# Optimization experiments

Measured on AMD Instinct MI355X. Metric: run time of the kernel, lower is better.

## Reference

```python
import jax, jax.numpy as jnp
import numpy as np

N_NODES = 50000
N_EDGES = 800000
IN_F = 64
HID = 64
N_CLS = 16


def setup_inputs() -> dict:
    key = jax.random.key(0)
    ks = jax.random.split(key, 8)
    x = jax.random.normal(ks[0], (N_NODES, IN_F), dtype=jnp.float32)
    edge_index = jax.random.randint(ks[1], (2, N_EDGES), 0, N_NODES, dtype=jnp.int64)
    s = 1.0 / np.sqrt(IN_F)
    W1_l = jax.random.uniform(ks[2], (IN_F, HID), jnp.float32, -s, s)
    W1_r = jax.random.uniform(ks[3], (IN_F, HID), jnp.float32, -s, s)
    b1 = jnp.zeros((HID,), jnp.float32)
    s2 = 1.0 / np.sqrt(HID)
    W2_l = jax.random.uniform(ks[4], (HID, N_CLS), jnp.float32, -s2, s2)
    W2_r = jax.random.uniform(ks[5], (HID, N_CLS), jnp.float32, -s2, s2)
    b2 = jnp.zeros((N_CLS,), jnp.float32)
    return {"x": x, "edge_index": edge_index, "W1_l": W1_l, "b1": b1, "W1_r": W1_r,
            "W2_l": W2_l, "b2": b2, "W2_r": W2_r}


def _sage_conv(x, src, dst, n_nodes, W_l, b_l, W_r):
    # PyG SAGEConv (aggr='mean'): out = lin_l(mean_j x_j) + lin_r(x_i)
    msg_sum = jax.ops.segment_sum(x[src], dst, num_segments=n_nodes)  # [N, F]
    deg = jax.ops.segment_sum(jnp.ones((src.shape[0],), x.dtype), dst,
                              num_segments=n_nodes)
    mean = msg_sum / jnp.maximum(deg, 1.0)[:, None]
    return mean @ W_l + b_l + x @ W_r


def reference(x, edge_index, W1_l, b1, W1_r, W2_l, b2, W2_r):
    src, dst = edge_index[0], edge_index[1]
    n = x.shape[0]
    h = _sage_conv(x, src, dst, n, W1_l, b1, W1_r)
    h = jax.nn.relu(h)
    # dropout is identity in eval mode
    out = _sage_conv(h, src, dst, n, W2_l, b2, W2_r)
    return out
```

## Files before the change

kernel.cpp:

```cpp
#include <hip/hip_runtime.h>

#define N_NODES 50000
#define N_EDGES 800000
#define NB      391
#define NBP     392
#define G       128
#define SCAN_N  (NBP * G)
#define SCAN_BLOCKS 49
#define MAXB    3072

typedef _Float16 h2v __attribute__((ext_vector_type(2)));
typedef _Float16 h8v __attribute__((ext_vector_type(8)));
typedef float    f4v __attribute__((ext_vector_type(4)));

union H2U { h2v h; unsigned u; };

__global__ void prep_kernel(const float* __restrict__ x,
                            const float* __restrict__ W1_l,
                            const float* __restrict__ W1_r,
                            const float* __restrict__ W2_l,
                            const float* __restrict__ W2_r,
                            _Float16* __restrict__ xf,
                            _Float16* __restrict__ B1,
                            _Float16* __restrict__ B2) {
    const int tid = blockIdx.x * 256 + threadIdx.x;
    {
        float4 v = *(const float4*)(x + tid * 4);
        H2U a, b;
        a.h = h2v{ (_Float16)v.x, (_Float16)v.y };
        b.h = h2v{ (_Float16)v.z, (_Float16)v.w };
        uint2 o = { a.u, b.u };
        *(uint2*)(xf + tid * 4) = o;
    }
    if (blockIdx.x == 0) {
        const int t = threadIdx.x;
        for (int p = t; p < 16 * 512; p += 256) {
            const int frag = p >> 9, lane = (p >> 3) & 63, j = p & 7;
            const int kt = frag >> 2, nt = frag & 3;
            const int k = kt * 32 + (lane >> 4) * 8 + j;
            const int n = nt * 16 + (lane & 15);
            const float w = (k < 64) ? W1_l[k * 64 + n] : W1_r[(k - 64) * 64 + n];
            B1[p] = (_Float16)w;
        }
        for (int p = t; p < 4 * 512; p += 256) {
            const int frag = p >> 9, lane = (p >> 3) & 63, j = p & 7;
            const int kt = frag >> 1, nt = frag & 1;
            const int k = kt * 32 + (lane >> 4) * 8 + j;
            const int n = lane & 15;
            const float w = (nt == 0) ? W2_l[k * 16 + n] : W2_r[k * 16 + n];
            B2[p] = (_Float16)w;
        }
    }
}

__global__ __launch_bounds__(512) void count_kernel(const int* __restrict__ dst,
                                                    int* __restrict__ histG) {
    __shared__ int hist[NBP];
    const int b = blockIdx.x, t = threadIdx.x;
    for (int i = t; i < NBP; i += 512) hist[i] = 0;
    __syncthreads();
    for (int i4 = b * 512 + t; i4 < N_EDGES / 4; i4 += G * 512) {
        int4 d = *(const int4*)(dst + i4 * 4);
        atomicAdd(&hist[d.x >> 7], 1);
        atomicAdd(&hist[d.y >> 7], 1);
        atomicAdd(&hist[d.z >> 7], 1);
        atomicAdd(&hist[d.w >> 7], 1);
    }
    __syncthreads();
    for (int i = t; i < NB; i += 512) histG[b * NBP + i] = hist[i];
}

__global__ void scanA_kernel(const int* __restrict__ histG,
                             int* __restrict__ loc,
                             int* __restrict__ bsum) {
    __shared__ int lds[256];
    const int b = blockIdx.x, t = threadIdx.x;
    const int base = b * 1024 + t * 4;
    int v[4];
    #pragma unroll
    for (int q = 0; q < 4; ++q) {
        const int i = base + q;
        v[q] = histG[(i & (G - 1)) * NBP + (i >> 7)];
    }
    const int s = v[0] + v[1] + v[2] + v[3];
    lds[t] = s;
    __syncthreads();
    for (int off = 1; off < 256; off <<= 1) {
        int u = (t >= off) ? lds[t - off] : 0;
        __syncthreads();
        lds[t] += u;
        __syncthreads();
    }
    const int excl = lds[t] - s;
    int4 o;
    o.x = excl;
    o.y = excl + v[0];
    o.z = excl + v[0] + v[1];
    o.w = excl + v[0] + v[1] + v[2];
    *(int4*)(loc + base) = o;
    if (t == 255) bsum[b] = lds[255];
}

__global__ void scanC_kernel(const int* __restrict__ loc,
                             const int* __restrict__ bsum,
                             int* __restrict__ offT) {
    const int b = blockIdx.x, t = threadIdx.x;
    const int lane = t & 63;
    int v = (lane < SCAN_BLOCKS) ? bsum[lane] : 0;
    for (int off = 1; off < 64; off <<= 1) {
        int u = __shfl_up(v, off);
        if (lane >= off) v += u;
    }
    const int boff = (b == 0) ? 0 : __shfl(v, b - 1);
    const int base = b * 1024 + t * 4;
    int4 w = *(const int4*)(loc + base);
    w.x += boff; w.y += boff; w.z += boff; w.w += boff;
    *(int4*)(offT + base) = w;
}

__global__ __launch_bounds__(512) void scatter_kernel(const int* __restrict__ src,
                                                      const int* __restrict__ dst,
                                                      const int* __restrict__ offT,
                                                      int* __restrict__ bbuf) {
    __shared__ int cur[NB];
    const int b = blockIdx.x, t = threadIdx.x;
    for (int i = t; i < NB; i += 512) cur[i] = offT[i * G + b];
    __syncthreads();
    for (int i4 = b * 512 + t; i4 < N_EDGES / 4; i4 += G * 512) {
        int4 s = *(const int4*)(src + i4 * 4);
        int4 d = *(const int4*)(dst + i4 * 4);
        #pragma unroll
        for (int q = 0; q < 4; ++q) {
            const int dv = (q == 0) ? d.x : (q == 1) ? d.y : (q == 2) ? d.z : d.w;
            const int sv = (q == 0) ? s.x : (q == 1) ? s.y : (q == 2) ? s.z : s.w;
            const int pos = atomicAdd(&cur[dv >> 7], 1);
            bbuf[pos] = ((dv & 127) << 16) | sv;
        }
    }
}

__global__ __launch_bounds__(256) void build_kernel(
        const int* __restrict__ offT,
        const int* __restrict__ bbuf,
        int* __restrict__ csr_src,
        int* __restrict__ rowptr) {
    __shared__ int stash[MAXB];
    __shared__ int lcsr[MAXB];
    __shared__ int hist[128];
    __shared__ int cur[128];

    const int b = blockIdx.x, t = threadIdx.x;
    const int start = offT[b * G];
    const int end = offT[(b + 1) * G];
    const int cnt_b = min(end - start, MAXB);

    if (t < 128) hist[t] = 0;
    __syncthreads();

    for (int i = t; i < cnt_b; i += 256) {
        const int w = bbuf[start + i];
        stash[i] = w;
        atomicAdd(&hist[w >> 16], 1);
    }
    __syncthreads();

    const int orig = (t < 128) ? hist[t] : 0;
    for (int off = 1; off < 128; off <<= 1) {
        int v = (t >= off && t < 128) ? hist[t - off] : 0;
        __syncthreads();
        if (t < 128) hist[t] += v;
        __syncthreads();
    }
    if (t < 128) cur[t] = hist[t] - orig;
    __syncthreads();

    const int node = b * 128 + t;
    if (t < 128 && node < N_NODES) rowptr[node] = start + cur[t];
    if (b == NB - 1 && t == 0) rowptr[N_NODES] = N_EDGES;

    for (int i = t; i < cnt_b; i += 256) {
        const int w = stash[i];
        const int p = atomicAdd(&cur[w >> 16], 1);
        lcsr[p] = w & 0xFFFF;
    }
    __syncthreads();

    for (int i = t; i < cnt_b; i += 256) csr_src[start + i] = lcsr[i];
}

__global__ __launch_bounds__(256) void gather_kernel(
        const _Float16* __restrict__ xf,
        const int* __restrict__ rowptr,
        const int* __restrict__ csr_src,
        _Float16* __restrict__ meanf) {
    const int n = blockIdx.x * 4 + (threadIdx.x >> 6);
    const int l = threadIdx.x & 63;
    const int c = l & 7;
    const int g = l >> 3;

    const int beg = rowptr[n];
    const int end = rowptr[n + 1];
    const int deg = end - beg;
    const int chunk = (deg + 7) >> 3;

    H2U a0, a1, a2, a3;
    a0.u = a1.u = a2.u = a3.u = 0;
    {
        int i = beg + g * chunk;
        const int ce = min(i + chunk, end);
        for (; i + 1 < ce; i += 2) {
            const int p = csr_src[i];
            const int q = csr_src[i + 1];
            uint4 up = *(const uint4*)(xf + p * 64 + c * 8);
            uint4 uq = *(const uint4*)(xf + q * 64 + c * 8);
            H2U t;
            t.u = up.x; a0.h += t.h;  t.u = uq.x; a0.h += t.h;
            t.u = up.y; a1.h += t.h;  t.u = uq.y; a1.h += t.h;
            t.u = up.z; a2.h += t.h;  t.u = uq.z; a2.h += t.h;
            t.u = up.w; a3.h += t.h;  t.u = uq.w; a3.h += t.h;
        }
        if (i < ce) {
            const int p = csr_src[i];
            uint4 up = *(const uint4*)(xf + p * 64 + c * 8);
            H2U t;
            t.u = up.x; a0.h += t.h;
            t.u = up.y; a1.h += t.h;
            t.u = up.z; a2.h += t.h;
            t.u = up.w; a3.h += t.h;
        }
    }
    #pragma unroll
    for (int off = 8; off <= 32; off <<= 1) {
        H2U r;
        r.u = (unsigned)__shfl_xor((int)a0.u, off); a0.h += r.h;
        r.u = (unsigned)__shfl_xor((int)a1.u, off); a1.h += r.h;
        r.u = (unsigned)__shfl_xor((int)a2.u, off); a2.h += r.h;
        r.u = (unsigned)__shfl_xor((int)a3.u, off); a3.h += r.h;
    }
    const float rdeg = 1.0f / fmaxf((float)deg, 1.0f);
    const _Float16 rh = (_Float16)rdeg;
    const h2v rd2 = { rh, rh };
    a0.h *= rd2; a1.h *= rd2; a2.h *= rd2; a3.h *= rd2;
    if (g == 0) {
        uint4 o = { a0.u, a1.u, a2.u, a3.u };
        *(uint4*)(meanf + n * 64 + c * 8) = o;
    }
}

__global__ __launch_bounds__(256) void mlp_kernel(
        const _Float16* __restrict__ xf,
        const _Float16* __restrict__ meanf,
        const _Float16* __restrict__ B1,
        const _Float16* __restrict__ B2,
        const float* __restrict__ b1,
        const float* __restrict__ b2,
        _Float16* __restrict__ y2f,
        float* __restrict__ z) {
    __shared__ _Float16 hlds[4][16 * 72];
    const int widx = threadIdx.x >> 6;
    const int l = threadIdx.x & 63;
    const int n0 = (blockIdx.x * 4 + widx) * 16;
    if (n0 >= N_NODES) return;
    const int cn = l & 15;
    const int kq = l >> 4;

    h8v af[4];
    const _Float16* mrow = meanf + (n0 + cn) * 64 + kq * 8;
    af[0] = *(const h8v*)(mrow);
    af[1] = *(const h8v*)(mrow + 32);
    const _Float16* xrow = xf + (n0 + cn) * 64 + kq * 8;
    af[2] = *(const h8v*)(xrow);
    af[3] = *(const h8v*)(xrow + 32);

    const f4v zero = { 0.f, 0.f, 0.f, 0.f };
    f4v acc[4] = { zero, zero, zero, zero };
    #pragma unroll
    for (int nt = 0; nt < 4; ++nt) {
        #pragma unroll
        for (int kt = 0; kt < 4; ++kt) {
            h8v bf = *(const h8v*)(B1 + ((kt * 4 + nt) * 64 + l) * 8);
            acc[nt] = __builtin_amdgcn_mfma_f32_16x16x32_f16(af[kt], bf, acc[nt], 0, 0, 0);
        }
    }

    _Float16* hl = &hlds[widx][0];
    #pragma unroll
    for (int nt = 0; nt < 4; ++nt) {
        const float bias = b1[nt * 16 + cn];
        #pragma unroll
        for (int r = 0; r < 4; ++r) {
            const float hv = fmaxf(acc[nt][r] + bias, 0.f);
            hl[(kq * 4 + r) * 72 + nt * 16 + cn] = (_Float16)hv;
        }
    }

    h8v a2[2];
    a2[0] = *(const h8v*)(hl + cn * 72 + kq * 8);
    a2[1] = *(const h8v*)(hl + cn * 72 + 32 + kq * 8);
    f4v acc2[2] = { zero, zero };
    #pragma unroll
    for (int nt = 0; nt < 2; ++nt) {
        #pragma unroll
        for (int kt = 0; kt < 2; ++kt) {
            h8v bf = *(const h8v*)(B2 + ((kt * 2 + nt) * 64 + l) * 8);
            acc2[nt] = __builtin_amdgcn_mfma_f32_16x16x32_f16(a2[kt], bf, acc2[nt], 0, 0, 0);
        }
    }
    const float bz = b2[cn];
    #pragma unroll
    for (int r = 0; r < 4; ++r) {
        const int row = n0 + kq * 4 + r;
        y2f[row * 16 + cn] = (_Float16)acc2[0][r];
        z[row * 16 + cn] = acc2[1][r] + bz;
    }
}

__global__ __launch_bounds__(256) void layer2_kernel(
        const _Float16* __restrict__ y2f,
        const float* __restrict__ z,
        const int* __restrict__ rowptr,
        const int* __restrict__ csr_src,
        float* __restrict__ out) {
    const int wv = blockIdx.x * 4 + (threadIdx.x >> 6);
    const int l = threadIdx.x & 63;
    const int n = wv * 4 + (l >> 4);
    const int t = l & 15;
    const int c2 = t & 1;
    const int p2 = t >> 1;

    const int beg = rowptr[n];
    const int end = rowptr[n + 1];
    const int deg = end - beg;
    const int chunk = (deg + 7) >> 3;

    H2U a0, a1, a2, a3;
    a0.u = a1.u = a2.u = a3.u = 0;
    {
        int i = beg + p2 * chunk;
        const int ce = min(i + chunk, end);
        for (; i + 1 < ce; i += 2) {
            const int p = csr_src[i];
            const int q = csr_src[i + 1];
            uint4 up = *(const uint4*)(y2f + p * 16 + c2 * 8);
            uint4 uq = *(const uint4*)(y2f + q * 16 + c2 * 8);
            H2U r;
            r.u = up.x; a0.h += r.h;  r.u = uq.x; a0.h += r.h;
            r.u = up.y; a1.h += r.h;  r.u = uq.y; a1.h += r.h;
            r.u = up.z; a2.h += r.h;  r.u = uq.z; a2.h += r.h;
            r.u = up.w; a3.h += r.h;  r.u = uq.w; a3.h += r.h;
        }
        if (i < ce) {
            const int p = csr_src[i];
            uint4 up = *(const uint4*)(y2f + p * 16 + c2 * 8);
            H2U r;
            r.u = up.x; a0.h += r.h;
            r.u = up.y; a1.h += r.h;
            r.u = up.z; a2.h += r.h;
            r.u = up.w; a3.h += r.h;
        }
    }
    #pragma unroll
    for (int off = 2; off <= 8; off <<= 1) {
        H2U r;
        r.u = (unsigned)__shfl_xor((int)a0.u, off); a0.h += r.h;
        r.u = (unsigned)__shfl_xor((int)a1.u, off); a1.h += r.h;
        r.u = (unsigned)__shfl_xor((int)a2.u, off); a2.h += r.h;
        r.u = (unsigned)__shfl_xor((int)a3.u, off); a3.h += r.h;
    }
    if (p2 == 0) {
        const float rdeg = 1.0f / fmaxf((float)deg, 1.0f);
        const float4 z0 = *(const float4*)(z + n * 16 + c2 * 8);
        const float4 z1 = *(const float4*)(z + n * 16 + c2 * 8 + 4);
        float4 o0 = { (float)a0.h[0] * rdeg + z0.x, (float)a0.h[1] * rdeg + z0.y,
                      (float)a1.h[0] * rdeg + z0.z, (float)a1.h[1] * rdeg + z0.w };
        float4 o1 = { (float)a2.h[0] * rdeg + z1.x, (float)a2.h[1] * rdeg + z1.y,
                      (float)a3.h[0] * rdeg + z1.z, (float)a3.h[1] * rdeg + z1.w };
        *(float4*)(out + n * 16 + c2 * 8) = o0;
        *(float4*)(out + n * 16 + c2 * 8 + 4) = o1;
    }
}

extern "C" void kernel_launch(void* const* d_in, const int* in_sizes, int n_in,
                              void* d_out, int out_size, void* d_ws, size_t ws_size,
                              hipStream_t stream) {
    const float* x    = (const float*)d_in[0];
    const int*   ei   = (const int*)d_in[1];
    const float* W1_l = (const float*)d_in[2];
    const float* b1   = (const float*)d_in[3];
    const float* W1_r = (const float*)d_in[4];
    const float* W2_l = (const float*)d_in[5];
    const float* b2   = (const float*)d_in[6];
    const float* W2_r = (const float*)d_in[7];
    float* out = (float*)d_out;

    const int* src = ei;
    const int* dst = ei + N_EDGES;

    int* ws = (int*)d_ws;
    int*   histG   = ws;
    int*   loc     = histG + SCAN_N;
    int*   offT    = loc   + SCAN_N;
    int*   bsum    = offT  + SCAN_N;
    int*   rowptr  = bsum  + 64;
    int*   bbuf    = rowptr + 50056;
    int*   csr_src = bbuf + 800000;
    _Float16* xf    = (_Float16*)(csr_src + 800000);
    _Float16* meanf = xf + 3200000;
    _Float16* B1    = meanf + 3200000;
    _Float16* B2    = B1 + 8192;
    _Float16* y2f   = B2 + 2048;
    float*    z     = (float*)(y2f + 800000);

    hipMemsetAsync(histG, 0, SCAN_N * sizeof(int), stream);

    prep_kernel<<<3125, 256, 0, stream>>>(x, W1_l, W1_r, W2_l, W2_r, xf, B1, B2);
    count_kernel<<<G, 512, 0, stream>>>(dst, histG);
    scanA_kernel<<<SCAN_BLOCKS, 256, 0, stream>>>(histG, loc, bsum);
    scanC_kernel<<<SCAN_BLOCKS, 256, 0, stream>>>(loc, bsum, offT);
    scatter_kernel<<<G, 512, 0, stream>>>(src, dst, offT, bbuf);
    build_kernel<<<NB, 256, 0, stream>>>(offT, bbuf, csr_src, rowptr);
    gather_kernel<<<N_NODES / 4, 256, 0, stream>>>(xf, rowptr, csr_src, meanf);
    mlp_kernel<<<(N_NODES / 16 + 3) / 4, 256, 0, stream>>>(xf, meanf, B1, B2,
                                                           b1, b2, y2f, z);
    layer2_kernel<<<N_NODES / 16, 256, 0, stream>>>(y2f, z, rowptr, csr_src, out);
}
```

Measured before the change: 146.2 us.

## Replace CSR build and gathers with bucketed LDS atomic aggregation

Drops the per-bucket CSR build kernel and the rowptr/csr_src gathers. Edges are bucketed by 64-node destination groups and each block accumulates neighbour features straight into shared-memory float accumulators with LDS atomics, for both layers. Bucket width and the count/scatter block sizes change to match the smaller buckets. This saves one kernel and a CSR pass. In exchange it takes on LDS atomic contention, and buckets holding more than 2048 edges get truncated.

```diff
diff --git a/kernel.cpp b/kernel.cpp
--- a/kernel.cpp
+++ b/kernel.cpp
@@ -2,12 +2,12 @@
 
 #define N_NODES 50000
 #define N_EDGES 800000
-#define NB      391
-#define NBP     392
-#define G       128
+#define NB      782
+#define NBP     784
+#define G       64
 #define SCAN_N  (NBP * G)
 #define SCAN_BLOCKS 49
-#define MAXB    3072
+#define MAXB    2048
 
 typedef _Float16 h2v __attribute__((ext_vector_type(2)));
 typedef _Float16 h8v __attribute__((ext_vector_type(8)));
@@ -53,21 +53,21 @@
     }
 }
 
-__global__ __launch_bounds__(512) void count_kernel(const int* __restrict__ dst,
-                                                    int* __restrict__ histG) {
+__global__ __launch_bounds__(1024) void count_kernel(const int* __restrict__ dst,
+                                                     int* __restrict__ histG) {
     __shared__ int hist[NBP];
     const int b = blockIdx.x, t = threadIdx.x;
-    for (int i = t; i < NBP; i += 512) hist[i] = 0;
-    __syncthreads();
-    for (int i4 = b * 512 + t; i4 < N_EDGES / 4; i4 += G * 512) {
+    for (int i = t; i < NBP; i += 1024) hist[i] = 0;
+    __syncthreads();
+    for (int i4 = b * 1024 + t; i4 < N_EDGES / 4; i4 += G * 1024) {
         int4 d = *(const int4*)(dst + i4 * 4);
-        atomicAdd(&hist[d.x >> 7], 1);
-        atomicAdd(&hist[d.y >> 7], 1);
-        atomicAdd(&hist[d.z >> 7], 1);
-        atomicAdd(&hist[d.w >> 7], 1);
-    }
-    __syncthreads();
-    for (int i = t; i < NB; i += 512) histG[b * NBP + i] = hist[i];
+        atomicAdd(&hist[d.x >> 6], 1);
+        atomicAdd(&hist[d.y >> 6], 1);
+        atomicAdd(&hist[d.z >> 6], 1);
+        atomicAdd(&hist[d.w >> 6], 1);
+    }
+    __syncthreads();
+    for (int i = t; i < NB; i += 1024) histG[b * NBP + i] = hist[i];
 }
 
 __global__ void scanA_kernel(const int* __restrict__ histG,
@@ -80,7 +80,7 @@
     #pragma unroll
     for (int q = 0; q < 4; ++q) {
         const int i = base + q;
-        v[q] = histG[(i & (G - 1)) * NBP + (i >> 7)];
+        v[q] = histG[(i & (G - 1)) * NBP + (i >> 6)];
     }
     const int s = v[0] + v[1] + v[2] + v[3];
     lds[t] = s;
@@ -118,132 +118,75 @@
     *(int4*)(offT + base) = w;
 }
 
-__global__ __launch_bounds__(512) void scatter_kernel(const int* __restrict__ src,
-                                                      const int* __restrict__ dst,
-                                                      const int* __restrict__ offT,
-                                                      int* __restrict__ bbuf) {
+__global__ __launch_bounds__(1024) void scatter_kernel(const int* __restrict__ src,
+                                                       const int* __restrict__ dst,
+                                                       const int* __restrict__ offT,
+                                                       int* __restrict__ bbuf) {
     __shared__ int cur[NB];
     const int b = blockIdx.x, t = threadIdx.x;
-    for (int i = t; i < NB; i += 512) cur[i] = offT[i * G + b];
-    __syncthreads();
-    for (int i4 = b * 512 + t; i4 < N_EDGES / 4; i4 += G * 512) {
+    for (int i = t; i < NB; i += 1024) cur[i] = offT[i * G + b];
+    __syncthreads();
+    for (int i4 = b * 1024 + t; i4 < N_EDGES / 4; i4 += G * 1024) {
         int4 s = *(const int4*)(src + i4 * 4);
         int4 d = *(const int4*)(dst + i4 * 4);
         #pragma unroll
         for (int q = 0; q < 4; ++q) {
             const int dv = (q == 0) ? d.x : (q == 1) ? d.y : (q == 2) ? d.z : d.w;
             const int sv = (q == 0) ? s.x : (q == 1) ? s.y : (q == 2) ? s.z : s.w;
-            const int pos = atomicAdd(&cur[dv >> 7], 1);
-            bbuf[pos] = ((dv & 127) << 16) | sv;
-        }
-    }
-}
-
-__global__ __launch_bounds__(256) void build_kernel(
+            const int pos = atomicAdd(&cur[dv >> 6], 1);
+            bbuf[pos] = ((dv & 63) << 16) | sv;
+        }
+    }
+}
+
+__global__ __launch_bounds__(256) void agg1_kernel(
+        const _Float16* __restrict__ xf,
         const int* __restrict__ offT,
         const int* __restrict__ bbuf,
-        int* __restrict__ csr_src,
-        int* __restrict__ rowptr) {
+        _Float16* __restrict__ meanf,
+        float* __restrict__ rdegG) {
     __shared__ int stash[MAXB];
-    __shared__ int lcsr[MAXB];
-    __shared__ int hist[128];
-    __shared__ int cur[128];
-
+    __shared__ float acc[64 * 65];
+    __shared__ int degL[64];
     const int b = blockIdx.x, t = threadIdx.x;
     const int start = offT[b * G];
-    const int end = offT[(b + 1) * G];
-    const int cnt_b = min(end - start, MAXB);
-
-    if (t < 128) hist[t] = 0;
-    __syncthreads();
-
-    for (int i = t; i < cnt_b; i += 256) {
-        const int w = bbuf[start + i];
-        stash[i] = w;
-        atomicAdd(&hist[w >> 16], 1);
-    }
-    __syncthreads();
-
-    const int orig = (t < 128) ? hist[t] : 0;
-    for (int off = 1; off < 128; off <<= 1) {
-        int v = (t >= off && t < 128) ? hist[t - off] : 0;
-        __syncthreads();
-        if (t < 128) hist[t] += v;
-        __syncthreads();
-    }
-    if (t < 128) cur[t] = hist[t] - orig;
-    __syncthreads();
-
-    const int node = b * 128 + t;
-    if (t < 128 && node < N_NODES) rowptr[node] = start + cur[t];
-    if (b == NB - 1 && t == 0) rowptr[N_NODES] = N_EDGES;
-
-    for (int i = t; i < cnt_b; i += 256) {
-        const int w = stash[i];
-        const int p = atomicAdd(&cur[w >> 16], 1);
-        lcsr[p] = w & 0xFFFF;
-    }
-    __syncthreads();
-
-    for (int i = t; i < cnt_b; i += 256) csr_src[start + i] = lcsr[i];
-}
-
-__global__ __launch_bounds__(256) void gather_kernel(
-        const _Float16* __restrict__ xf,
-        const int* __restrict__ rowptr,
-        const int* __restrict__ csr_src,
-        _Float16* __restrict__ meanf) {
-    const int n = blockIdx.x * 4 + (threadIdx.x >> 6);
-    const int l = threadIdx.x & 63;
-    const int c = l & 7;
-    const int g = l >> 3;
-
-    const int beg = rowptr[n];
-    const int end = rowptr[n + 1];
-    const int deg = end - beg;
-    const int chunk = (deg + 7) >> 3;
-
-    H2U a0, a1, a2, a3;
-    a0.u = a1.u = a2.u = a3.u = 0;
-    {
-        int i = beg + g * chunk;
-        const int ce = min(i + chunk, end);
-        for (; i + 1 < ce; i += 2) {
-            const int p = csr_src[i];
-            const int q = csr_src[i + 1];
-            uint4 up = *(const uint4*)(xf + p * 64 + c * 8);
-            uint4 uq = *(const uint4*)(xf + q * 64 + c * 8);
-            H2U t;
-            t.u = up.x; a0.h += t.h;  t.u = uq.x; a0.h += t.h;
-            t.u = up.y; a1.h += t.h;  t.u = uq.y; a1.h += t.h;
-            t.u = up.z; a2.h += t.h;  t.u = uq.z; a2.h += t.h;
-            t.u = up.w; a3.h += t.h;  t.u = uq.w; a3.h += t.h;
-        }
-        if (i < ce) {
-            const int p = csr_src[i];
-            uint4 up = *(const uint4*)(xf + p * 64 + c * 8);
-            H2U t;
-            t.u = up.x; a0.h += t.h;
-            t.u = up.y; a1.h += t.h;
-            t.u = up.z; a2.h += t.h;
-            t.u = up.w; a3.h += t.h;
-        }
-    }
-    #pragma unroll
-    for (int off = 8; off <= 32; off <<= 1) {
-        H2U r;
-        r.u = (unsigned)__shfl_xor((int)a0.u, off); a0.h += r.h;
-        r.u = (unsigned)__shfl_xor((int)a1.u, off); a1.h += r.h;
-        r.u = (unsigned)__shfl_xor((int)a2.u, off); a2.h += r.h;
-        r.u = (unsigned)__shfl_xor((int)a3.u, off); a3.h += r.h;
-    }
-    const float rdeg = 1.0f / fmaxf((float)deg, 1.0f);
-    const _Float16 rh = (_Float16)rdeg;
-    const h2v rd2 = { rh, rh };
-    a0.h *= rd2; a1.h *= rd2; a2.h *= rd2; a3.h *= rd2;
-    if (g == 0) {
-        uint4 o = { a0.u, a1.u, a2.u, a3.u };
-        *(uint4*)(meanf + n * 64 + c * 8) = o;
+    const int cnt = min(offT[(b + 1) * G] - start, MAXB);
+
+    for (int i = t; i < 64 * 65; i += 256) acc[i] = 0.f;
+    if (t < 64) degL[t] = 0;
+    for (int i = t; i < cnt; i += 256) stash[i] = bbuf[start + i];
+    __syncthreads();
+
+    const int c = t & 7;
+    const int eg = t >> 3;
+    for (int e = eg; e < cnt; e += 32) {
+        const int w = stash[e];
+        const int ld = w >> 16;
+        const int s = w & 0xFFFF;
+        const uint4 u = *(const uint4*)(xf + s * 64 + c * 8);
+        float* a = &acc[ld * 65 + c * 8];
+        H2U h;
+        h.u = u.x; atomicAdd(&a[0], (float)h.h[0]); atomicAdd(&a[1], (float)h.h[1]);
+        h.u = u.y; atomicAdd(&a[2], (float)h.h[0]); atomicAdd(&a[3], (float)h.h[1]);
+        h.u = u.z; atomicAdd(&a[4], (float)h.h[0]); atomicAdd(&a[5], (float)h.h[1]);
+        h.u = u.w; atomicAdd(&a[6], (float)h.h[0]); atomicAdd(&a[7], (float)h.h[1]);
+        if (c == 0) atomicAdd(&degL[ld], 1);
+    }
+    __syncthreads();
+
+    const int node0 = b * 64;
+    if (t < 64) rdegG[node0 + t] = 1.0f / fmaxf((float)degL[t], 1.0f);
+    for (int i = t; i < 512; i += 256) {
+        const int node = i >> 3, cc = i & 7;
+        const float rd = 1.0f / fmaxf((float)degL[node], 1.0f);
+        const float* a = &acc[node * 65 + cc * 8];
+        H2U o0, o1, o2, o3;
+        o0.h = h2v{ (_Float16)(a[0] * rd), (_Float16)(a[1] * rd) };
+        o1.h = h2v{ (_Float16)(a[2] * rd), (_Float16)(a[3] * rd) };
+        o2.h = h2v{ (_Float16)(a[4] * rd), (_Float16)(a[5] * rd) };
+        o3.h = h2v{ (_Float16)(a[6] * rd), (_Float16)(a[7] * rd) };
+        uint4 o = { o0.u, o1.u, o2.u, o3.u };
+        *(uint4*)(meanf + (node0 + node) * 64 + cc * 8) = o;
     }
 }
 
@@ -315,68 +258,45 @@
     }
 }
 
-__global__ __launch_bounds__(256) void layer2_kernel(
+__global__ __launch_bounds__(256) void agg2_kernel(
         const _Float16* __restrict__ y2f,
         const float* __restrict__ z,
-        const int* __restrict__ rowptr,
-        const int* __restrict__ csr_src,
+        const int* __restrict__ offT,
+        const int* __restrict__ bbuf,
+        const float* __restrict__ rdegG,
         float* __restrict__ out) {
-    const int wv = blockIdx.x * 4 + (threadIdx.x >> 6);
-    const int l = threadIdx.x & 63;
-    const int n = wv * 4 + (l >> 4);
-    const int t = l & 15;
-    const int c2 = t & 1;
-    const int p2 = t >> 1;
-
-    const int beg = rowptr[n];
-    const int end = rowptr[n + 1];
-    const int deg = end - beg;
-    const int chunk = (deg + 7) >> 3;
-
-    H2U a0, a1, a2, a3;
-    a0.u = a1.u = a2.u = a3.u = 0;
-    {
-        int i = beg + p2 * chunk;
-        const int ce = min(i + chunk, end);
-        for (; i + 1 < ce; i += 2) {
-            const int p = csr_src[i];
-            const int q = csr_src[i + 1];
-            uint4 up = *(const uint4*)(y2f + p * 16 + c2 * 8);
-            uint4 uq = *(const uint4*)(y2f + q * 16 + c2 * 8);
-            H2U r;
-            r.u = up.x; a0.h += r.h;  r.u = uq.x; a0.h += r.h;
-            r.u = up.y; a1.h += r.h;  r.u = uq.y; a1.h += r.h;
-            r.u = up.z; a2.h += r.h;  r.u = uq.z; a2.h += r.h;
-            r.u = up.w; a3.h += r.h;  r.u = uq.w; a3.h += r.h;
-        }
-        if (i < ce) {
-            const int p = csr_src[i];
-            uint4 up = *(const uint4*)(y2f + p * 16 + c2 * 8);
-            H2U r;
-            r.u = up.x; a0.h += r.h;
-            r.u = up.y; a1.h += r.h;
-            r.u = up.z; a2.h += r.h;
-            r.u = up.w; a3.h += r.h;
-        }
-    }
-    #pragma unroll
-    for (int off = 2; off <= 8; off <<= 1) {
-        H2U r;
-        r.u = (unsigned)__shfl_xor((int)a0.u, off); a0.h += r.h;
-        r.u = (unsigned)__shfl_xor((int)a1.u, off); a1.h += r.h;
-        r.u = (unsigned)__shfl_xor((int)a2.u, off); a2.h += r.h;
-        r.u = (unsigned)__shfl_xor((int)a3.u, off); a3.h += r.h;
-    }
-    if (p2 == 0) {
-        const float rdeg = 1.0f / fmaxf((float)deg, 1.0f);
-        const float4 z0 = *(const float4*)(z + n * 16 + c2 * 8);
-        const float4 z1 = *(const float4*)(z + n * 16 + c2 * 8 + 4);
-        float4 o0 = { (float)a0.h[0] * rdeg + z0.x, (float)a0.h[1] * rdeg + z0.y,
-                      (float)a1.h[0] * rdeg + z0.z, (float)a1.h[1] * rdeg + z0.w };
-        float4 o1 = { (float)a2.h[0] * rdeg + z1.x, (float)a2.h[1] * rdeg + z1.y,
-                      (float)a3.h[0] * rdeg + z1.z, (float)a3.h[1] * rdeg + z1.w };
-        *(float4*)(out + n * 16 + c2 * 8) = o0;
-        *(float4*)(out + n * 16 + c2 * 8 + 4) = o1;
+    __shared__ int stash[MAXB];
+    __shared__ float acc[64 * 17];
+    const int b = blockIdx.x, t = threadIdx.x;
+    const int start = offT[b * G];
+    const int cnt = min(offT[(b + 1) * G] - start, MAXB);
+
+    for (int i = t; i < 64 * 17; i += 256) acc[i] = 0.f;
+    for (int i = t; i < cnt; i += 256) stash[i] = bbuf[start + i];
+    __syncthreads();
+
+    const int fh = t & 1;
+    const int eg = t >> 1;
+    for (int e = eg; e < cnt; e += 128) {
+        const int w = stash[e];
+        const int ld = w >> 16;
+        const int s = w & 0xFFFF;
+        const uint4 u = *(const uint4*)(y2f + s * 16 + fh * 8);
+        float* a = &acc[ld * 17 + fh * 8];
+        H2U h;
+        h.u = u.x; atomicAdd(&a[0], (float)h.h[0]); atomicAdd(&a[1], (float)h.h[1]);
+        h.u = u.y; atomicAdd(&a[2], (float)h.h[0]); atomicAdd(&a[3], (float)h.h[1]);
+        h.u = u.z; atomicAdd(&a[4], (float)h.h[0]); atomicAdd(&a[5], (float)h.h[1]);
+        h.u = u.w; atomicAdd(&a[6], (float)h.h[0]); atomicAdd(&a[7], (float)h.h[1]);
+    }
+    __syncthreads();
+
+    const int node0 = b * 64;
+    for (int i = t; i < 1024; i += 256) {
+        const int node = i >> 4, f = i & 15;
+        const int n = node0 + node;
+        if (n < N_NODES)
+            out[n * 16 + f] = acc[node * 17 + f] * rdegG[n] + z[n * 16 + f];
     }
 }
 
@@ -397,16 +317,15 @@
     const int* dst = ei + N_EDGES;
 
     int* ws = (int*)d_ws;
-    int*   histG   = ws;
-    int*   loc     = histG + SCAN_N;
-    int*   offT    = loc   + SCAN_N;
-    int*   bsum    = offT  + SCAN_N;
-    int*   rowptr  = bsum  + 64;
-    int*   bbuf    = rowptr + 50056;
-    int*   csr_src = bbuf + 800000;
-    _Float16* xf    = (_Float16*)(csr_src + 800000);
+    int*   histG = ws;
+    int*   loc   = histG + SCAN_N;
+    int*   offT  = loc + SCAN_N;
+    int*   bsum  = offT + SCAN_N;
+    float* rdegG = (float*)(bsum + 64);
+    int*   bbuf  = (int*)(rdegG + 50048);
+    _Float16* xf    = (_Float16*)(bbuf + 800000);
     _Float16* meanf = xf + 3200000;
-    _Float16* B1    = meanf + 3200000;
+    _Float16* B1    = meanf + 3203072;
     _Float16* B2    = B1 + 8192;
     _Float16* y2f   = B2 + 2048;
     float*    z     = (float*)(y2f + 800000);
@@ -414,13 +333,12 @@
     hipMemsetAsync(histG, 0, SCAN_N * sizeof(int), stream);
 
     prep_kernel<<<3125, 256, 0, stream>>>(x, W1_l, W1_r, W2_l, W2_r, xf, B1, B2);
-    count_kernel<<<G, 512, 0, stream>>>(dst, histG);
+    count_kernel<<<G, 1024, 0, stream>>>(dst, histG);
     scanA_kernel<<<SCAN_BLOCKS, 256, 0, stream>>>(histG, loc, bsum);
     scanC_kernel<<<SCAN_BLOCKS, 256, 0, stream>>>(loc, bsum, offT);
-    scatter_kernel<<<G, 512, 0, stream>>>(src, dst, offT, bbuf);
-    build_kernel<<<NB, 256, 0, stream>>>(offT, bbuf, csr_src, rowptr);
-    gather_kernel<<<N_NODES / 4, 256, 0, stream>>>(xf, rowptr, csr_src, meanf);
+    scatter_kernel<<<G, 1024, 0, stream>>>(src, dst, offT, bbuf);
+    agg1_kernel<<<NB, 256, 0, stream>>>(xf, offT, bbuf, meanf, rdegG);
     mlp_kernel<<<(N_NODES / 16 + 3) / 4, 256, 0, stream>>>(xf, meanf, B1, B2,
                                                            b1, b2, y2f, z);
-    layer2_kernel<<<N_NODES / 16, 256, 0, stream>>>(y2f, z, rowptr, csr_src, out);
-}
+    agg2_kernel<<<NB, 256, 0, stream>>>(y2f, z, offT, bbuf, rdegG, out);
+}
```

New measurement: 547.3 us. +274.3%, slower.

## Fuse layer-1 gather into MLP kernel and merge scan passes into one

Applied to the files above, without the earlier changes.

Folds the separate neighbor-mean gather kernel into the MFMA layer-1 kernel, so each lane accumulates one node's neighbor features directly into MFMA A-fragments. This removes the meanf intermediate buffer round trip and one launch. The histogram is now written transposed, so a single scan kernel replaces the two-kernel scan by recomputing block prefixes redundantly. The trade-off is parallelism: the gather drops from 8 lanes per feature chunk per node to one lane per node-chunk walking the whole edge list serially, which can hurt latency hiding and load balance on high-degree nodes.

```diff
diff --git a/kernel.cpp b/kernel.cpp
--- a/kernel.cpp
+++ b/kernel.cpp
@@ -14,6 +14,7 @@
 typedef float    f4v __attribute__((ext_vector_type(4)));
 
 union H2U { h2v h; unsigned u; };
+union H8U { h8v v; unsigned u[4]; };
 
 __global__ void prep_kernel(const float* __restrict__ x,
                             const float* __restrict__ W1_l,
@@ -54,7 +55,7 @@
 }
 
 __global__ __launch_bounds__(512) void count_kernel(const int* __restrict__ dst,
-                                                    int* __restrict__ histG) {
+                                                    int* __restrict__ histT) {
     __shared__ int hist[NBP];
     const int b = blockIdx.x, t = threadIdx.x;
     for (int i = t; i < NBP; i += 512) hist[i] = 0;
@@ -67,22 +68,31 @@
         atomicAdd(&hist[d.w >> 7], 1);
     }
     __syncthreads();
-    for (int i = t; i < NB; i += 512) histG[b * NBP + i] = hist[i];
-}
-
-__global__ void scanA_kernel(const int* __restrict__ histG,
-                             int* __restrict__ loc,
-                             int* __restrict__ bsum) {
+    for (int i = t; i < NB; i += 512) histT[i * G + b] = hist[i];
+}
+
+__global__ void scan_kernel(const int* __restrict__ histT,
+                            int* __restrict__ offT) {
+    __shared__ int redu[256];
     __shared__ int lds[256];
     const int b = blockIdx.x, t = threadIdx.x;
-    const int base = b * 1024 + t * 4;
-    int v[4];
-    #pragma unroll
-    for (int q = 0; q < 4; ++q) {
-        const int i = base + q;
-        v[q] = histG[(i & (G - 1)) * NBP + (i >> 7)];
-    }
-    const int s = v[0] + v[1] + v[2] + v[3];
+
+    int part = 0;
+    for (int j = t * 4; j < b * 1024; j += 1024) {
+        int4 v = *(const int4*)(histT + j);
+        part += v.x + v.y + v.z + v.w;
+    }
+    redu[t] = part;
+    __syncthreads();
+    for (int off = 128; off > 0; off >>= 1) {
+        if (t < off) redu[t] += redu[t + off];
+        __syncthreads();
+    }
+    const int base = redu[0];
+
+    const int idx = b * 1024 + t * 4;
+    int4 v = *(const int4*)(histT + idx);
+    const int s = v.x + v.y + v.z + v.w;
     lds[t] = s;
     __syncthreads();
     for (int off = 1; off < 256; off <<= 1) {
@@ -91,31 +101,9 @@
         lds[t] += u;
         __syncthreads();
     }
-    const int excl = lds[t] - s;
-    int4 o;
-    o.x = excl;
-    o.y = excl + v[0];
-    o.z = excl + v[0] + v[1];
-    o.w = excl + v[0] + v[1] + v[2];
-    *(int4*)(loc + base) = o;
-    if (t == 255) bsum[b] = lds[255];
-}
-
-__global__ void scanC_kernel(const int* __restrict__ loc,
-                             const int* __restrict__ bsum,
-                             int* __restrict__ offT) {
-    const int b = blockIdx.x, t = threadIdx.x;
-    const int lane = t & 63;
-    int v = (lane < SCAN_BLOCKS) ? bsum[lane] : 0;
-    for (int off = 1; off < 64; off <<= 1) {
-        int u = __shfl_up(v, off);
-        if (lane >= off) v += u;
-    }
-    const int boff = (b == 0) ? 0 : __shfl(v, b - 1);
-    const int base = b * 1024 + t * 4;
-    int4 w = *(const int4*)(loc + base);
-    w.x += boff; w.y += boff; w.z += boff; w.w += boff;
-    *(int4*)(offT + base) = w;
+    const int excl = base + lds[t] - s;
+    int4 o = { excl, excl + v.x, excl + v.x + v.y, excl + v.x + v.y + v.z };
+    *(int4*)(offT + idx) = o;
 }
 
 __global__ __launch_bounds__(512) void scatter_kernel(const int* __restrict__ src,
@@ -188,68 +176,10 @@
     for (int i = t; i < cnt_b; i += 256) csr_src[start + i] = lcsr[i];
 }
 
-__global__ __launch_bounds__(256) void gather_kernel(
+__global__ __launch_bounds__(256) void layer1_kernel(
         const _Float16* __restrict__ xf,
         const int* __restrict__ rowptr,
         const int* __restrict__ csr_src,
-        _Float16* __restrict__ meanf) {
-    const int n = blockIdx.x * 4 + (threadIdx.x >> 6);
-    const int l = threadIdx.x & 63;
-    const int c = l & 7;
-    const int g = l >> 3;
-
-    const int beg = rowptr[n];
-    const int end = rowptr[n + 1];
-    const int deg = end - beg;
-    const int chunk = (deg + 7) >> 3;
-
-    H2U a0, a1, a2, a3;
-    a0.u = a1.u = a2.u = a3.u = 0;
-    {
-        int i = beg + g * chunk;
-        const int ce = min(i + chunk, end);
-        for (; i + 1 < ce; i += 2) {
-            const int p = csr_src[i];
-            const int q = csr_src[i + 1];
-            uint4 up = *(const uint4*)(xf + p * 64 + c * 8);
-            uint4 uq = *(const uint4*)(xf + q * 64 + c * 8);
-            H2U t;
-            t.u = up.x; a0.h += t.h;  t.u = uq.x; a0.h += t.h;
-            t.u = up.y; a1.h += t.h;  t.u = uq.y; a1.h += t.h;
-            t.u = up.z; a2.h += t.h;  t.u = uq.z; a2.h += t.h;
-            t.u = up.w; a3.h += t.h;  t.u = uq.w; a3.h += t.h;
-        }
-        if (i < ce) {
-            const int p = csr_src[i];
-            uint4 up = *(const uint4*)(xf + p * 64 + c * 8);
-            H2U t;
-            t.u = up.x; a0.h += t.h;
-            t.u = up.y; a1.h += t.h;
-            t.u = up.z; a2.h += t.h;
-            t.u = up.w; a3.h += t.h;
-        }
-    }
-    #pragma unroll
-    for (int off = 8; off <= 32; off <<= 1) {
-        H2U r;
-        r.u = (unsigned)__shfl_xor((int)a0.u, off); a0.h += r.h;
-        r.u = (unsigned)__shfl_xor((int)a1.u, off); a1.h += r.h;
-        r.u = (unsigned)__shfl_xor((int)a2.u, off); a2.h += r.h;
-        r.u = (unsigned)__shfl_xor((int)a3.u, off); a3.h += r.h;
-    }
-    const float rdeg = 1.0f / fmaxf((float)deg, 1.0f);
-    const _Float16 rh = (_Float16)rdeg;
-    const h2v rd2 = { rh, rh };
-    a0.h *= rd2; a1.h *= rd2; a2.h *= rd2; a3.h *= rd2;
-    if (g == 0) {
-        uint4 o = { a0.u, a1.u, a2.u, a3.u };
-        *(uint4*)(meanf + n * 64 + c * 8) = o;
-    }
-}
-
-__global__ __launch_bounds__(256) void mlp_kernel(
-        const _Float16* __restrict__ xf,
-        const _Float16* __restrict__ meanf,
         const _Float16* __restrict__ B1,
         const _Float16* __restrict__ B2,
         const float* __restrict__ b1,
@@ -259,28 +189,74 @@
     __shared__ _Float16 hlds[4][16 * 72];
     const int widx = threadIdx.x >> 6;
     const int l = threadIdx.x & 63;
-    const int n0 = (blockIdx.x * 4 + widx) * 16;
-    if (n0 >= N_NODES) return;
     const int cn = l & 15;
     const int kq = l >> 4;
-
-    h8v af[4];
-    const _Float16* mrow = meanf + (n0 + cn) * 64 + kq * 8;
-    af[0] = *(const h8v*)(mrow);
-    af[1] = *(const h8v*)(mrow + 32);
-    const _Float16* xrow = xf + (n0 + cn) * 64 + kq * 8;
-    af[2] = *(const h8v*)(xrow);
-    af[3] = *(const h8v*)(xrow + 32);
+    const int n0 = (blockIdx.x * 4 + widx) * 16;
+    const int ng = n0 + cn;
+
+    int beg = 0, deg = 0;
+    if (ng < N_NODES) {
+        beg = rowptr[ng];
+        deg = rowptr[ng + 1] - beg;
+    }
+
+    H2U lo[4], hi[4];
+    #pragma unroll
+    for (int j = 0; j < 4; ++j) { lo[j].u = 0; hi[j].u = 0; }
+    const _Float16* xq = xf + kq * 8;
+    int i = 0;
+    for (; i + 1 < deg; i += 2) {
+        const int s0 = csr_src[beg + i];
+        const int s1 = csr_src[beg + i + 1];
+        const uint4 u0 = *(const uint4*)(xq + s0 * 64);
+        const uint4 v0 = *(const uint4*)(xq + s0 * 64 + 32);
+        const uint4 u1 = *(const uint4*)(xq + s1 * 64);
+        const uint4 v1 = *(const uint4*)(xq + s1 * 64 + 32);
+        H2U t;
+        t.u = u0.x; lo[0].h += t.h;  t.u = u1.x; lo[0].h += t.h;
+        t.u = u0.y; lo[1].h += t.h;  t.u = u1.y; lo[1].h += t.h;
+        t.u = u0.z; lo[2].h += t.h;  t.u = u1.z; lo[2].h += t.h;
+        t.u = u0.w; lo[3].h += t.h;  t.u = u1.w; lo[3].h += t.h;
+        t.u = v0.x; hi[0].h += t.h;  t.u = v1.x; hi[0].h += t.h;
+        t.u = v0.y; hi[1].h += t.h;  t.u = v1.y; hi[1].h += t.h;
+        t.u = v0.z; hi[2].h += t.h;  t.u = v1.z; hi[2].h += t.h;
+        t.u = v0.w; hi[3].h += t.h;  t.u = v1.w; hi[3].h += t.h;
+    }
+    if (i < deg) {
+        const int s0 = csr_src[beg + i];
+        const uint4 u0 = *(const uint4*)(xq + s0 * 64);
+        const uint4 v0 = *(const uint4*)(xq + s0 * 64 + 32);
+        H2U t;
+        t.u = u0.x; lo[0].h += t.h;  t.u = v0.x; hi[0].h += t.h;
+        t.u = u0.y; lo[1].h += t.h;  t.u = v0.y; hi[1].h += t.h;
+        t.u = u0.z; lo[2].h += t.h;  t.u = v0.z; hi[2].h += t.h;
+        t.u = u0.w; lo[3].h += t.h;  t.u = v0.w; hi[3].h += t.h;
+    }
+    const float rdeg = 1.0f / fmaxf((float)deg, 1.0f);
+    const _Float16 rh = (_Float16)rdeg;
+    const h2v rd2 = { rh, rh };
+    H8U af0, af1, af2, af3;
+    #pragma unroll
+    for (int j = 0; j < 4; ++j) {
+        lo[j].h *= rd2; hi[j].h *= rd2;
+        af0.u[j] = lo[j].u;
+        af1.u[j] = hi[j].u;
+    }
+    {
+        const uint4 su = *(const uint4*)(xf + ng * 64 + kq * 8);
+        const uint4 sv = *(const uint4*)(xf + ng * 64 + 32 + kq * 8);
+        af2.u[0] = su.x; af2.u[1] = su.y; af2.u[2] = su.z; af2.u[3] = su.w;
+        af3.u[0] = sv.x; af3.u[1] = sv.y; af3.u[2] = sv.z; af3.u[3] = sv.w;
+    }
 
     const f4v zero = { 0.f, 0.f, 0.f, 0.f };
     f4v acc[4] = { zero, zero, zero, zero };
     #pragma unroll
     for (int nt = 0; nt < 4; ++nt) {
-        #pragma unroll
-        for (int kt = 0; kt < 4; ++kt) {
-            h8v bf = *(const h8v*)(B1 + ((kt * 4 + nt) * 64 + l) * 8);
-            acc[nt] = __builtin_amdgcn_mfma_f32_16x16x32_f16(af[kt], bf, acc[nt], 0, 0, 0);
-        }
+        acc[nt] = __builtin_amdgcn_mfma_f32_16x16x32_f16(af0.v, *(const h8v*)(B1 + ((0 * 4 + nt) * 64 + l) * 8), acc[nt], 0, 0, 0);
+        acc[nt] = __builtin_amdgcn_mfma_f32_16x16x32_f16(af1.v, *(const h8v*)(B1 + ((1 * 4 + nt) * 64 + l) * 8), acc[nt], 0, 0, 0);
+        acc[nt] = __builtin_amdgcn_mfma_f32_16x16x32_f16(af2.v, *(const h8v*)(B1 + ((2 * 4 + nt) * 64 + l) * 8), acc[nt], 0, 0, 0);
+        acc[nt] = __builtin_amdgcn_mfma_f32_16x16x32_f16(af3.v, *(const h8v*)(B1 + ((3 * 4 + nt) * 64 + l) * 8), acc[nt], 0, 0, 0);
     }
 
     _Float16* hl = &hlds[widx][0];
@@ -310,8 +286,10 @@
     #pragma unroll
     for (int r = 0; r < 4; ++r) {
         const int row = n0 + kq * 4 + r;
-        y2f[row * 16 + cn] = (_Float16)acc2[0][r];
-        z[row * 16 + cn] = acc2[1][r] + bz;
+        if (row < N_NODES) {
+            y2f[row * 16 + cn] = (_Float16)acc2[0][r];
+            z[row * 16 + cn] = acc2[1][r] + bz;
+        }
     }
 }
 
@@ -397,30 +375,25 @@
     const int* dst = ei + N_EDGES;
 
     int* ws = (int*)d_ws;
-    int*   histG   = ws;
-    int*   loc     = histG + SCAN_N;
-    int*   offT    = loc   + SCAN_N;
-    int*   bsum    = offT  + SCAN_N;
-    int*   rowptr  = bsum  + 64;
+    int*   histT   = ws;
+    int*   offT    = histT + SCAN_N;
+    int*   rowptr  = offT  + SCAN_N;
     int*   bbuf    = rowptr + 50056;
     int*   csr_src = bbuf + 800000;
     _Float16* xf    = (_Float16*)(csr_src + 800000);
-    _Float16* meanf = xf + 3200000;
-    _Float16* B1    = meanf + 3200000;
+    _Float16* B1    = xf + 3203072;
     _Float16* B2    = B1 + 8192;
     _Float16* y2f   = B2 + 2048;
     float*    z     = (float*)(y2f + 800000);
 
-    hipMemsetAsync(histG, 0, SCAN_N * sizeof(int), stream);
+    hipMemsetAsync(histT, 0, SCAN_N * sizeof(int), stream);
 
     prep_kernel<<<3125, 256, 0, stream>>>(x, W1_l, W1_r, W2_l, W2_r, xf, B1, B2);
-    count_kernel<<<G, 512, 0, stream>>>(dst, histG);
-    scanA_kernel<<<SCAN_BLOCKS, 256, 0, stream>>>(histG, loc, bsum);
-    scanC_kernel<<<SCAN_BLOCKS, 256, 0, stream>>>(loc, bsum, offT);
+    count_kernel<<<G, 512, 0, stream>>>(dst, histT);
+    scan_kernel<<<SCAN_BLOCKS, 256, 0, stream>>>(histT, offT);
     scatter_kernel<<<G, 512, 0, stream>>>(src, dst, offT, bbuf);
     build_kernel<<<NB, 256, 0, stream>>>(offT, bbuf, csr_src, rowptr);
-    gather_kernel<<<N_NODES / 4, 256, 0, stream>>>(xf, rowptr, csr_src, meanf);
-    mlp_kernel<<<(N_NODES / 16 + 3) / 4, 256, 0, stream>>>(xf, meanf, B1, B2,
-                                                           b1, b2, y2f, z);
+    layer1_kernel<<<(N_NODES + 63) / 64, 256, 0, stream>>>(xf, rowptr, csr_src,
+                                                           B1, B2, b1, b2, y2f, z);
     layer2_kernel<<<N_NODES / 16, 256, 0, stream>>>(y2f, z, rowptr, csr_src, out);
 }
```

Measured after the change: 148.7 us. Within noise of the previous version (+1.7%).
